# Kernel optimization log

Measured on AMD Instinct MI355X. Metric: run time of the kernel, lower is better.

## Reference

```python
import jax, jax.numpy as jnp
import numpy as np

B, DX, DS, H, K, NSN = 1048576, 32, 16, 128, 64, 4

def setup_inputs() -> dict:
    key = jax.random.key(0)
    ks = jax.random.split(key, 9)
    return {
        "x": jax.random.normal(ks[0], (B, DX), jnp.float32),
        "s": jax.random.normal(ks[1], (B, DS), jnp.float32),
        "hidden": jax.random.normal(ks[2], (B, H), jnp.float32),
        "naive_pred": jax.random.normal(ks[3], (B, 1), jnp.float32),
        # learned parameters
        "centers": jax.random.normal(ks[4], (K, DX), jnp.float32),
        "W_tune": jax.random.normal(ks[5], (H, 1), jnp.float32) * 0.05,
        "b_tune": jnp.zeros((1,), jnp.float32),
        "W_sn": jax.random.normal(ks[6], (NSN, K, DS), jnp.float32) * 0.1,
        "b_sn": jax.random.normal(ks[7], (NSN, K), jnp.float32) * 0.1,
        "running_sn_weight": jnp.full((K, NSN), 1.0 / NSN, jnp.float32),
    }

def reference(x, s, hidden, naive_pred, centers, W_tune, b_tune, W_sn, b_sn, running_sn_weight):
    # tune head: linear -> sigmoid, [B,1]
    x_tune = jax.nn.sigmoid(hidden @ W_tune + b_tune)
    # nearest-centroid clustering: argmin ||x - c_k||^2 (||x||^2 dropped, constant per row)
    dist = jnp.sum(centers * centers, axis=1) - 2.0 * (x @ centers.T)  # [B,K]
    x_cluster = jnp.argmin(dist, axis=1)  # [B] int32
    # sub-networks: per-cluster linear heads on s; gather cluster-indexed weights
    Ws = W_sn[:, x_cluster, :]                                   # [NSN,B,DS] gather
    x_sn = jnp.einsum('nbd,bd->bn', Ws, s) + b_sn[:, x_cluster].T  # [B,NSN]
    # indexed weighted reduction over sub-network outputs
    w = running_sn_weight[x_cluster]                             # [B,NSN] gather
    x_sn_sum = jnp.sum(x_sn * w, axis=1, keepdims=True)          # [B,1]
    out = x_sn_sum + x_tune * (naive_pred - x_sn_sum)
    return out
```

## Files before the change

kernel.cpp:

```cpp
#include <hip/hip_runtime.h>
#include <math.h>

#define DXc 32
#define DSc 16
#define Hc  128
#define Kc  64
#define NSNc 4

__global__ __launch_bounds__(256, 4) void snclust_fused(
    const float* __restrict__ x,
    const float* __restrict__ s,
    const float* __restrict__ hidden,
    const float* __restrict__ naive_pred,
    const float* __restrict__ centers,
    const float* __restrict__ W_tune,
    const float* __restrict__ b_tune,
    const float* __restrict__ W_sn,
    const float* __restrict__ b_sn,
    const float* __restrict__ rsw,
    float* __restrict__ out,
    int n)
{
    __shared__ float sWc[Kc][DSc + 1];
    __shared__ float sbc[Kc];
    __shared__ float sc2[Kc];

    const int tid = threadIdx.x;

    for (int e = tid; e < Kc * DSc; e += 256) {
        const int c = e >> 4;
        const int j = e & 15;
        float acc = 0.f;
#pragma unroll
        for (int nn = 0; nn < NSNc; ++nn)
            acc = fmaf(rsw[c * NSNc + nn], W_sn[(nn * Kc + c) * DSc + j], acc);
        sWc[c][j] = acc;
    }
    if (tid < Kc) {
        const int c = tid;
        float accb = 0.f;
#pragma unroll
        for (int nn = 0; nn < NSNc; ++nn)
            accb = fmaf(rsw[c * NSNc + nn], b_sn[nn * Kc + c], accb);
        sbc[c] = accb;
        float c2 = 0.f;
#pragma unroll
        for (int d = 0; d < DXc; ++d) {
            const float cv = centers[c * DXc + d];
            c2 = fmaf(cv, cv, c2);
        }
        sc2[c] = c2;
    }
    __syncthreads();

    const int b = blockIdx.x * 256 + tid;
    if (b >= n) return;

    float xr[DXc];
    {
        const float4* x4 = reinterpret_cast<const float4*>(x + (size_t)b * DXc);
#pragma unroll
        for (int i = 0; i < DXc / 4; ++i) {
            const float4 v = x4[i];
            xr[i * 4 + 0] = v.x;
            xr[i * 4 + 1] = v.y;
            xr[i * 4 + 2] = v.z;
            xr[i * 4 + 3] = v.w;
        }
    }

    float hacc = 0.f;
    {
        const float4* h4 = reinterpret_cast<const float4*>(hidden + (size_t)b * Hc);
#pragma unroll 8
        for (int i = 0; i < Hc / 4; ++i) {
            const float4 v = h4[i];
            hacc = fmaf(v.x, W_tune[i * 4 + 0], hacc);
            hacc = fmaf(v.y, W_tune[i * 4 + 1], hacc);
            hacc = fmaf(v.z, W_tune[i * 4 + 2], hacc);
            hacc = fmaf(v.w, W_tune[i * 4 + 3], hacc);
        }
    }
    const float z = hacc + b_tune[0];
    const float x_tune = 1.0f / (1.0f + __expf(-z));

    int bestk = 0;
    float bestd = INFINITY;
#pragma unroll 2
    for (int k = 0; k < Kc; ++k) {
        float dot = 0.f;
#pragma unroll
        for (int d = 0; d < DXc; ++d)
            dot = fmaf(xr[d], centers[k * DXc + d], dot);
        const float dist = fmaf(-2.0f, dot, sc2[k]);
        if (dist < bestd) { bestd = dist; bestk = k; }
    }

    float snacc = sbc[bestk];
    {
        const float4* s4 = reinterpret_cast<const float4*>(s + (size_t)b * DSc);
#pragma unroll
        for (int i = 0; i < DSc / 4; ++i) {
            const float4 v = s4[i];
            snacc = fmaf(v.x, sWc[bestk][i * 4 + 0], snacc);
            snacc = fmaf(v.y, sWc[bestk][i * 4 + 1], snacc);
            snacc = fmaf(v.z, sWc[bestk][i * 4 + 2], snacc);
            snacc = fmaf(v.w, sWc[bestk][i * 4 + 3], snacc);
        }
    }

    const float np_ = naive_pred[b];
    out[b] = snacc + x_tune * (np_ - snacc);
}

extern "C" void kernel_launch(void* const* d_in, const int* in_sizes, int n_in,
                              void* d_out, int out_size, void* d_ws, size_t ws_size,
                              hipStream_t stream) {
    const float* x          = (const float*)d_in[0];
    const float* s          = (const float*)d_in[1];
    const float* hidden     = (const float*)d_in[2];
    const float* naive_pred = (const float*)d_in[3];
    const float* centers    = (const float*)d_in[4];
    const float* W_tune     = (const float*)d_in[5];
    const float* b_tune     = (const float*)d_in[6];
    const float* W_sn       = (const float*)d_in[7];
    const float* b_sn       = (const float*)d_in[8];
    const float* rsw        = (const float*)d_in[9];
    float* out = (float*)d_out;

    const int n = in_sizes[3];
    const int blocks = (n + 255) / 256;
    snclust_fused<<<blocks, 256, 0, stream>>>(x, s, hidden, naive_pred, centers,
                                              W_tune, b_tune, W_sn, b_sn, rsw,
                                              out, n);
}
```

Before: 157.7 us.

## Stage x, hidden and s through padded LDS for fully coalesced global loads

Result: slower. 163.9 us (+4.0%).

```diff
diff --git a/kernel.cpp b/kernel.cpp
--- a/kernel.cpp
+++ b/kernel.cpp
@@ -7,7 +7,13 @@
 #define Kc  64
 #define NSNc 4
 
-__global__ __launch_bounds__(256, 4) void snclust_fused(
+union SMemU {
+    float4 sx[256 * 9];
+    float4 shid[64 * 33];
+    float4 ss[256 * 5];
+};
+
+__global__ __launch_bounds__(256, 3) void snclust_fused(
     const float* __restrict__ x,
     const float* __restrict__ s,
     const float* __restrict__ hidden,
@@ -21,11 +27,15 @@
     float* __restrict__ out,
     int n)
 {
+    __shared__ SMemU sm;
     __shared__ float sWc[Kc][DSc + 1];
     __shared__ float sbc[Kc];
     __shared__ float sc2[Kc];
+    __shared__ float shdot[256];
+    __shared__ float spart[64][5];
 
     const int tid = threadIdx.x;
+    const size_t blockBase = (size_t)blockIdx.x * 256;
 
     for (int e = tid; e < Kc * DSc; e += 256) {
         const int c = e >> 4;
@@ -53,25 +63,119 @@
     }
     __syncthreads();
 
-    const int b = blockIdx.x * 256 + tid;
-    if (b >= n) return;
-
-    float xr[DXc];
-    {
-        const float4* x4 = reinterpret_cast<const float4*>(x + (size_t)b * DXc);
+    if (blockBase + 256 <= (size_t)n) {
+
+        {
+            const float4* gx = reinterpret_cast<const float4*>(x) + blockBase * 8;
+#pragma unroll
+            for (int i = 0; i < 8; ++i) {
+                const int f = i * 256 + tid;
+                sm.sx[(f >> 3) * 9 + (f & 7)] = gx[f];
+            }
+        }
+        __syncthreads();
+        float xr[DXc];
+#pragma unroll
+        for (int i = 0; i < 8; ++i) {
+            const float4 v = sm.sx[tid * 9 + i];
+            xr[i * 4 + 0] = v.x; xr[i * 4 + 1] = v.y;
+            xr[i * 4 + 2] = v.z; xr[i * 4 + 3] = v.w;
+        }
+        __syncthreads();
+
+        {
+            const float4* gh = reinterpret_cast<const float4*>(hidden) + blockBase * 32;
+            const int r   = tid & 63;
+            const int seg = __builtin_amdgcn_readfirstlane(tid >> 6);
+            for (int c = 0; c < 4; ++c) {
+#pragma unroll
+                for (int i = 0; i < 8; ++i) {
+                    const int f = i * 256 + tid;
+                    sm.shid[(f >> 5) * 33 + (f & 31)] = gh[c * 2048 + f];
+                }
+                __syncthreads();
+                float a0 = 0.f, a1 = 0.f;
+                const int base = r * 33 + seg * 8;
+#pragma unroll
+                for (int j = 0; j < 4; ++j) {
+                    const float4 v = sm.shid[base + 2 * j];
+                    const float4 w = sm.shid[base + 2 * j + 1];
+                    const int wb = seg * 32 + j * 8;
+                    a0 = fmaf(v.x, W_tune[wb + 0], a0);
+                    a0 = fmaf(v.y, W_tune[wb + 1], a0);
+                    a0 = fmaf(v.z, W_tune[wb + 2], a0);
+                    a0 = fmaf(v.w, W_tune[wb + 3], a0);
+                    a1 = fmaf(w.x, W_tune[wb + 4], a1);
+                    a1 = fmaf(w.y, W_tune[wb + 5], a1);
+                    a1 = fmaf(w.z, W_tune[wb + 6], a1);
+                    a1 = fmaf(w.w, W_tune[wb + 7], a1);
+                }
+                spart[r][seg] = a0 + a1;
+                __syncthreads();
+                if (tid < 64)
+                    shdot[c * 64 + tid] =
+                        (spart[tid][0] + spart[tid][1]) + (spart[tid][2] + spart[tid][3]);
+            }
+        }
+        __syncthreads();
+        const float hacc = shdot[tid];
+        const float z = hacc + b_tune[0];
+        const float x_tune = 1.0f / (1.0f + __expf(-z));
+
+        float4 st[4];
+        {
+            const float4* gs = reinterpret_cast<const float4*>(s) + blockBase * 4;
+#pragma unroll
+            for (int i = 0; i < 4; ++i)
+                st[i] = gs[i * 256 + tid];
+        }
+        const float np_ = naive_pred[blockBase + tid];
+
+        int bestk = 0;
+        float bestd = INFINITY;
+#pragma unroll 2
+        for (int k = 0; k < Kc; ++k) {
+            float dot = 0.f;
+#pragma unroll
+            for (int d = 0; d < DXc; ++d)
+                dot = fmaf(xr[d], centers[k * DXc + d], dot);
+            const float dist = fmaf(-2.0f, dot, sc2[k]);
+            if (dist < bestd) { bestd = dist; bestk = k; }
+        }
+
+#pragma unroll
+        for (int i = 0; i < 4; ++i) {
+            const int f = i * 256 + tid;
+            sm.ss[(f >> 2) * 5 + (f & 3)] = st[i];
+        }
+        __syncthreads();
+
+        float snacc = sbc[bestk];
+#pragma unroll
+        for (int i = 0; i < 4; ++i) {
+            const float4 v = sm.ss[tid * 5 + i];
+            snacc = fmaf(v.x, sWc[bestk][i * 4 + 0], snacc);
+            snacc = fmaf(v.y, sWc[bestk][i * 4 + 1], snacc);
+            snacc = fmaf(v.z, sWc[bestk][i * 4 + 2], snacc);
+            snacc = fmaf(v.w, sWc[bestk][i * 4 + 3], snacc);
+        }
+        out[blockBase + tid] = snacc + x_tune * (np_ - snacc);
+
+    } else {
+        const size_t b = blockBase + tid;
+        if (b >= (size_t)n) return;
+
+        float xr[DXc];
+        const float4* x4 = reinterpret_cast<const float4*>(x + b * DXc);
 #pragma unroll
         for (int i = 0; i < DXc / 4; ++i) {
             const float4 v = x4[i];
-            xr[i * 4 + 0] = v.x;
-            xr[i * 4 + 1] = v.y;
-            xr[i * 4 + 2] = v.z;
-            xr[i * 4 + 3] = v.w;
-        }
-    }
-
-    float hacc = 0.f;
-    {
-        const float4* h4 = reinterpret_cast<const float4*>(hidden + (size_t)b * Hc);
+            xr[i * 4 + 0] = v.x; xr[i * 4 + 1] = v.y;
+            xr[i * 4 + 2] = v.z; xr[i * 4 + 3] = v.w;
+        }
+
+        float hacc = 0.f;
+        const float4* h4 = reinterpret_cast<const float4*>(hidden + b * Hc);
 #pragma unroll 8
         for (int i = 0; i < Hc / 4; ++i) {
             const float4 v = h4[i];
@@ -80,25 +184,23 @@
             hacc = fmaf(v.z, W_tune[i * 4 + 2], hacc);
             hacc = fmaf(v.w, W_tune[i * 4 + 3], hacc);
         }
-    }
-    const float z = hacc + b_tune[0];
-    const float x_tune = 1.0f / (1.0f + __expf(-z));
-
-    int bestk = 0;
-    float bestd = INFINITY;
+        const float z = hacc + b_tune[0];
+        const float x_tune = 1.0f / (1.0f + __expf(-z));
+
+        int bestk = 0;
+        float bestd = INFINITY;
 #pragma unroll 2
-    for (int k = 0; k < Kc; ++k) {
-        float dot = 0.f;
-#pragma unroll
-        for (int d = 0; d < DXc; ++d)
-            dot = fmaf(xr[d], centers[k * DXc + d], dot);
-        const float dist = fmaf(-2.0f, dot, sc2[k]);
-        if (dist < bestd) { bestd = dist; bestk = k; }
-    }
-
-    float snacc = sbc[bestk];
-    {
-        const float4* s4 = reinterpret_cast<const float4*>(s + (size_t)b * DSc);
+        for (int k = 0; k < Kc; ++k) {
+            float dot = 0.f;
+#pragma unroll
+            for (int d = 0; d < DXc; ++d)
+                dot = fmaf(xr[d], centers[k * DXc + d], dot);
+            const float dist = fmaf(-2.0f, dot, sc2[k]);
+            if (dist < bestd) { bestd = dist; bestk = k; }
+        }
+
+        float snacc = sbc[bestk];
+        const float4* s4 = reinterpret_cast<const float4*>(s + b * DSc);
 #pragma unroll
         for (int i = 0; i < DSc / 4; ++i) {
             const float4 v = s4[i];
@@ -107,10 +209,9 @@
             snacc = fmaf(v.z, sWc[bestk][i * 4 + 2], snacc);
             snacc = fmaf(v.w, sWc[bestk][i * 4 + 3], snacc);
         }
+        const float np_ = naive_pred[b];
+        out[b] = snacc + x_tune * (np_ - snacc);
     }
-
-    const float np_ = naive_pred[b];
-    out[b] = snacc + x_tune * (np_ - snacc);
 }
 
 extern "C" void kernel_launch(void* const* d_in, const int* in_sizes, int n_in,
```
